# Kernel optimization log

Hardware: AMD Instinct MI355X
Metric: run time of the kernel (lower is better)

## Reference

```python
import jax, jax.numpy as jnp
import numpy as np

INTRA_W, TYPE_W, INTER_W = 1.0, 0.5, 0.5
MARGIN, TAU, EPS = 1.0, 0.1, 1e-8
N, D = 200000, 256          # nodes, feature dim
NT, EPT = 4, 2048           # n types, edges per type
E = NT * EPT                # 8192 hyperedges
SAMP_PER_TYPE = 100         # max_edges_per_type for intra loss
MAX_PAIRS = 500             # inter-loss pair sample


def setup_inputs() -> dict:
    key = jax.random.key(0)
    k1, k2, k3, k4, k5 = jax.random.split(key, 5)
    z_nodes = jax.random.normal(k1, (N, D), dtype=jnp.float32)
    # deterministic variable edge sizes in [8, 56]
    sizes = 8 + (np.arange(E) * 7919) % 49
    M = int(sizes.sum())  # 262128
    member_edge_id = jnp.asarray(np.repeat(np.arange(E), sizes), dtype=jnp.int32)
    member_node_idx = jax.random.randint(k2, (M,), 0, N, dtype=jnp.int32)
    edge_type = jnp.asarray(np.repeat(np.arange(NT), EPT), dtype=jnp.int32)
    # intra-loss edge sampling: 100 edges per type (mimics torch.randperm sampling)
    perm = jax.random.permutation(k3, EPT)
    intra_sample = jnp.concatenate(
        [perm[:SAMP_PER_TYPE] + t * EPT for t in range(NT)]).astype(jnp.int32)
    # inter-loss pair sampling (mimics torch.randint + self-collision fixup)
    pair_idx1 = jax.random.randint(k4, (MAX_PAIRS,), 0, E, dtype=jnp.int32)
    pair_idx2 = jax.random.randint(k5, (MAX_PAIRS,), 0, E, dtype=jnp.int32)
    pair_idx2 = jnp.where(pair_idx1 == pair_idx2, (pair_idx2 + 1) % E, pair_idx2)
    return dict(z_nodes=z_nodes, member_node_idx=member_node_idx,
                member_edge_id=member_edge_id, edge_type=edge_type,
                intra_sample=intra_sample, pair_idx1=pair_idx1, pair_idx2=pair_idx2)


def reference(z_nodes, member_node_idx, member_edge_id, edge_type,
              intra_sample, pair_idx1, pair_idx2):
    # --- ragged segment mean: hyperedge embeddings ---
    gathered = z_nodes[member_node_idx]                               # [M, D]
    counts = jax.ops.segment_sum(jnp.ones_like(member_edge_id, jnp.float32),
                                 member_edge_id, num_segments=E)      # [E]
    edge_sum = jax.ops.segment_sum(gathered, member_edge_id, num_segments=E)
    edge_emb = edge_sum / counts[:, None]                             # [E, D]

    # --- B1: intra-hyperedge loss over sampled edges ---
    sq_dist = jnp.sum((gathered - edge_emb[member_edge_id]) ** 2, axis=-1)  # [M]
    per_edge = jax.ops.segment_sum(sq_dist, member_edge_id, num_segments=E) / counts
    intra = jnp.mean(per_edge[intra_sample])

    # --- B2: type contrastive InfoNCE ---
    z = edge_emb / jnp.linalg.norm(edge_emb, axis=-1, keepdims=True)  # [E, D]
    sim = jnp.matmul(z, z.T) / TAU                                    # [E, E]
    self_mask = jnp.eye(E, dtype=bool)
    exp_sim = jnp.exp(sim) * (~self_mask)
    denom = exp_sim.sum(axis=1)
    type_mask = (edge_type[None, :] == edge_type[:, None]) & ~self_mask
    numer = jnp.sum(exp_sim * type_mask, axis=1)
    per_row = -jnp.log((numer + EPS) / (denom + EPS))
    has_pos = type_mask.sum(axis=1) > 0
    type_loss = jnp.sum(jnp.where(has_pos, per_row, 0.0)) / jnp.maximum(
        has_pos.sum().astype(per_row.dtype), 1.0)

    # --- B3: inter-hyperedge margin loss on sampled pairs ---
    dist = jnp.linalg.norm(edge_emb[pair_idx1] - edge_emb[pair_idx2], axis=-1)
    inter = jnp.mean(jax.nn.relu(MARGIN - dist) ** 2)

    total = INTRA_W * intra + TYPE_W * type_loss + INTER_W * inter
    return jnp.stack([intra, type_loss, inter, total])
```

## Files before the change

### kernel.cpp

```cpp
#include <hip/hip_runtime.h>


#define DDIM 256
#define NTYPES 4
#define TAU_INV 10.0f
#define EPSV 1e-8f

#define ROWS_PER_BLOCK 128
#define ROWS_PER_WAVE 32
#define CHUNK 1024
#define CTILE 64
#define BPAD 264

typedef short v8s __attribute__((ext_vector_type(8)));
typedef float v4f __attribute__((ext_vector_type(4)));
typedef unsigned short ushort_t;

__device__ __forceinline__ int lower_bound_i(const int* __restrict__ a, int n, int key) {
  int lo = 0, hi = n;
  while (lo < hi) { int mid = (lo + hi) >> 1; if (a[mid] < key) lo = mid + 1; else hi = mid; }
  return lo;
}

__device__ __forceinline__ ushort_t f2bf(float f) {
  union { float f; unsigned u; } v; v.f = f;
  unsigned r = v.u + 0x7FFFu + ((v.u >> 16) & 1u);
  return (ushort_t)(r >> 16);
}

__global__ __launch_bounds__(256)
void edge_kernel(const float* __restrict__ z, const int* __restrict__ mni,
                 const int* __restrict__ mei, int M, int E,
                 ushort_t* __restrict__ zn, float* __restrict__ emb,
                 float* __restrict__ per_edge, float* __restrict__ typeSums,
                 float* __restrict__ selfArr, float* __restrict__ scalars) {
  __shared__ int shIdx[64];
  __shared__ float shAcc[1024];
  __shared__ float shRed[12];
  int e = blockIdx.x;
  int tid = threadIdx.x;
  if (tid < NTYPES) typeSums[e * NTYPES + tid] = 0.f;
  if (tid == NTYPES) selfArr[e] = 0.f;
  if (e == 0 && tid >= 16 && tid < 24) scalars[tid - 16] = 0.f;

  int s = lower_bound_i(mei, M, e);
  int t = lower_bound_i(mei, M, e + 1);
  int cnt = t - s;
  if (tid < cnt) shIdx[tid] = mni[s + tid];
  __syncthreads();

  int group = tid >> 6, lane = tid & 63;
  float4 acc = make_float4(0.f, 0.f, 0.f, 0.f);
  float sq = 0.f;
  int m = group;
  for (; m + 4 < cnt; m += 8) {
    int n0 = shIdx[m], n1 = shIdx[m + 4];
    float4 v0 = *(const float4*)(z + (size_t)n0 * DDIM + lane * 4);
    float4 v1 = *(const float4*)(z + (size_t)n1 * DDIM + lane * 4);
    acc.x += v0.x; acc.y += v0.y; acc.z += v0.z; acc.w += v0.w;
    sq += v0.x * v0.x + v0.y * v0.y + v0.z * v0.z + v0.w * v0.w;
    acc.x += v1.x; acc.y += v1.y; acc.z += v1.z; acc.w += v1.w;
    sq += v1.x * v1.x + v1.y * v1.y + v1.z * v1.z + v1.w * v1.w;
  }
  if (m < cnt) {
    int n0 = shIdx[m];
    float4 v0 = *(const float4*)(z + (size_t)n0 * DDIM + lane * 4);
    acc.x += v0.x; acc.y += v0.y; acc.z += v0.z; acc.w += v0.w;
    sq += v0.x * v0.x + v0.y * v0.y + v0.z * v0.z + v0.w * v0.w;
  }

  *(float4*)(&shAcc[tid * 4]) = acc;
  __syncthreads();
  int d = tid;
  float total = shAcc[d] + shAcc[256 + d] + shAcc[512 + d] + shAcc[768 + d];
  float inv = 1.0f / (float)cnt;
  float mu = total * inv;
  emb[(size_t)e * DDIM + d] = mu;

  float a1 = sq, a2 = mu * mu;
  #pragma unroll
  for (int off = 32; off > 0; off >>= 1) {
    a1 += __shfl_down(a1, off);
    a2 += __shfl_down(a2, off);
  }
  if (lane == 0) { shRed[group] = a1; shRed[4 + group] = a2; }
  __syncthreads();
  if (tid == 0) {
    float sqT = shRed[0] + shRed[1] + shRed[2] + shRed[3];
    float musqT = shRed[4] + shRed[5] + shRed[6] + shRed[7];
    per_edge[e] = sqT * inv - musqT;
    shRed[8] = musqT;
  }
  __syncthreads();
  float rn = rsqrtf(shRed[8]);
  zn[(size_t)e * DDIM + d] = f2bf(mu * rn);
}

__global__ __launch_bounds__(256)
void gemm_kernel(const ushort_t* __restrict__ zn, const int* __restrict__ edge_type,
                 int E, float* __restrict__ typeSums, float* __restrict__ selfArr) {
  __shared__ __align__(16) ushort_t sB[CTILE * BPAD];

  int tid = threadIdx.x;
  int lane = tid & 63, wave = tid >> 6;
  int quad = lane >> 4, l15 = lane & 15;
  int rb = blockIdx.y;
  int cb = blockIdx.x;
  int row0 = rb * ROWS_PER_BLOCK + wave * ROWS_PER_WAVE;
  int c0 = cb * CHUNK;
  int T = edge_type[c0];

  v8s aF[2][8];
  #pragma unroll
  for (int rt = 0; rt < 2; ++rt) {
    const ushort_t* base = zn + (size_t)(row0 + rt * 16 + l15) * DDIM + quad * 8;
    #pragma unroll
    for (int ks = 0; ks < 8; ++ks)
      aF[rt][ks] = *(const v8s*)(base + ks * 32);
  }

  float acc[2][4] = {};

  for (int tile = 0; tile < CHUNK / CTILE; ++tile) {
    int col0 = c0 + tile * CTILE;
    #pragma unroll
    for (int it = 0; it < 8; ++it) {
      int flat = it * 256 + tid;
      int r = flat >> 5;
      int c8 = flat & 31;
      *(v8s*)(&sB[r * BPAD + c8 * 8]) =
          *(const v8s*)(zn + (size_t)(col0 + r) * DDIM + c8 * 8);
    }
    __syncthreads();

    v4f c[2][4];
    #pragma unroll
    for (int rt = 0; rt < 2; ++rt)
      #pragma unroll
      for (int ct = 0; ct < 4; ++ct)
        c[rt][ct] = (v4f){0.f, 0.f, 0.f, 0.f};

    #pragma unroll
    for (int ks = 0; ks < 8; ++ks) {
      v8s a0 = aF[0][ks], a1 = aF[1][ks];
      #pragma unroll
      for (int ct = 0; ct < 4; ++ct) {
        v8s b = *(const v8s*)(&sB[(ct * 16 + l15) * BPAD + ks * 32 + quad * 8]);
        c[0][ct] = __builtin_amdgcn_mfma_f32_16x16x32_bf16(a0, b, c[0][ct], 0, 0, 0);
        c[1][ct] = __builtin_amdgcn_mfma_f32_16x16x32_bf16(a1, b, c[1][ct], 0, 0, 0);
      }
    }

    #pragma unroll
    for (int rt = 0; rt < 2; ++rt) {
      #pragma unroll
      for (int ct = 0; ct < 4; ++ct) {
        int col = col0 + ct * 16 + l15;
        #pragma unroll
        for (int r = 0; r < 4; ++r) {
          int row = row0 + rt * 16 + quad * 4 + r;
          float ev = __expf(c[rt][ct][r] * TAU_INV);
          if (col == row) selfArr[row] = ev;
          acc[rt][r] += ev;
        }
      }
    }
    __syncthreads();
  }

  #pragma unroll
  for (int rt = 0; rt < 2; ++rt) {
    #pragma unroll
    for (int r = 0; r < 4; ++r) {
      float v = acc[rt][r];
      v += __shfl_xor(v, 1);
      v += __shfl_xor(v, 2);
      v += __shfl_xor(v, 4);
      v += __shfl_xor(v, 8);
      if (l15 == 0) {
        int row = row0 + rt * 16 + quad * 4 + r;
        atomicAdd(&typeSums[row * NTYPES + T], v);
      }
    }
  }
}

__global__ __launch_bounds__(256)
void small_kernel(const float* __restrict__ emb, const float* __restrict__ per_edge,
                  const int* __restrict__ intra_sample, int nIntra,
                  const int* __restrict__ p1, const int* __restrict__ p2, int nPairs,
                  float* __restrict__ scalars) {
  __shared__ float sh[4];
  int b = blockIdx.x;
  int tid = threadIdx.x;
  int lane = tid & 63, wave = tid >> 6;
  int nPairBlocks = (nPairs + 3) >> 2;
  if (b < nPairBlocks) {
    int p = b * 4 + wave;
    if (p < nPairs) {
      int i1 = p1[p], i2 = p2[p];
      const float4* r1 = (const float4*)(emb + (size_t)i1 * DDIM);
      const float4* r2 = (const float4*)(emb + (size_t)i2 * DDIM);
      float4 x = r1[lane], y = r2[lane];
      float d0 = x.x - y.x, d1 = x.y - y.y, d2 = x.z - y.z, d3 = x.w - y.w;
      float s = d0 * d0 + d1 * d1 + d2 * d2 + d3 * d3;
      #pragma unroll
      for (int off = 32; off > 0; off >>= 1) s += __shfl_down(s, off);
      if (lane == 0) {
        float dist = sqrtf(s);
        float v = fmaxf(1.0f - dist, 0.0f);
        atomicAdd(&scalars[1], v * v);
      }
    }
  } else if (b == nPairBlocks) {
    float s = 0.f;
    for (int i = tid; i < nIntra; i += 256) s += per_edge[intra_sample[i]];
    #pragma unroll
    for (int off = 32; off > 0; off >>= 1) s += __shfl_down(s, off);
    if (lane == 0) sh[wave] = s;
    __syncthreads();
    if (tid == 0) atomicAdd(&scalars[0], sh[0] + sh[1] + sh[2] + sh[3]);
  }
}

__global__ __launch_bounds__(256)
void rowloss_kernel(const float* __restrict__ typeSums, const float* __restrict__ selfArr,
                    const int* __restrict__ edge_type, int E, float* __restrict__ scalars) {
  __shared__ float sh[8];
  int tid = threadIdx.x;
  int row = blockIdx.x * 256 + tid;
  float pr = 0.f, hp = 0.f;
  if (row < E) {
    int t = edge_type[row];
    float self = selfArr[row];
    float s0 = typeSums[row * 4 + 0];
    float s1 = typeSums[row * 4 + 1];
    float s2 = typeSums[row * 4 + 2];
    float s3 = typeSums[row * 4 + 3];
    float denom = (s0 + s1 + s2 + s3) - self;
    float own = (t == 0) ? s0 : (t == 1) ? s1 : (t == 2) ? s2 : s3;
    float numer = own - self;
    int cs = lower_bound_i(edge_type, E, t);
    int ce = lower_bound_i(edge_type, E, t + 1);
    if (ce - cs - 1 > 0) {
      hp = 1.f;
      pr = -__logf((numer + EPSV) / (denom + EPSV));
    }
  }
  float a1 = pr, a2 = hp;
  #pragma unroll
  for (int off = 32; off > 0; off >>= 1) {
    a1 += __shfl_down(a1, off);
    a2 += __shfl_down(a2, off);
  }
  int wid = tid >> 6, lane = tid & 63;
  if (lane == 0) { sh[wid] = a1; sh[4 + wid] = a2; }
  __syncthreads();
  if (tid == 0) {
    atomicAdd(&scalars[2], sh[0] + sh[1] + sh[2] + sh[3]);
    atomicAdd(&scalars[3], sh[4] + sh[5] + sh[6] + sh[7]);
  }
}

__global__ void finalize_kernel(const float* __restrict__ scalars, int nIntra, int nPairs,
                                float* __restrict__ out) {
  if (threadIdx.x == 0) {
    float intra = scalars[0] / (float)nIntra;
    float inter = scalars[1] / (float)nPairs;
    float typeL = scalars[2] / fmaxf(scalars[3], 1.f);
    out[0] = intra;
    out[1] = typeL;
    out[2] = inter;
    out[3] = 1.0f * intra + 0.5f * typeL + 0.5f * inter;
  }
}

extern "C" void kernel_launch(void* const* d_in, const int* in_sizes, int n_in,
                              void* d_out, int out_size, void* d_ws, size_t ws_size,
                              hipStream_t stream) {
  const float* z      = (const float*)d_in[0];
  const int* mni      = (const int*)d_in[1];
  const int* mei      = (const int*)d_in[2];
  const int* etype    = (const int*)d_in[3];
  const int* intra_s  = (const int*)d_in[4];
  const int* p1       = (const int*)d_in[5];
  const int* p2       = (const int*)d_in[6];
  int M      = in_sizes[1];
  int E      = in_sizes[3];
  int nIntra = in_sizes[4];
  int nPairs = in_sizes[5];

  char* ws = (char*)d_ws;
  ushort_t* zn   = (ushort_t*)ws;
  float* emb     = (float*)(ws + (size_t)E * DDIM * 2);
  float* per_edge = (float*)(ws + (size_t)E * DDIM * 6);
  float* typeSums = per_edge + E;
  float* selfArr  = typeSums + (size_t)E * NTYPES;
  float* scalars  = selfArr + E;

  float* out = (float*)d_out;

  edge_kernel<<<E, 256, 0, stream>>>(z, mni, mei, M, E, zn, emb, per_edge,
                                     typeSums, selfArr, scalars);

  dim3 g(E / CHUNK, E / ROWS_PER_BLOCK);
  gemm_kernel<<<g, 256, 0, stream>>>(zn, etype, E, typeSums, selfArr);

  int nPB = (nPairs + 3) / 4;
  small_kernel<<<nPB + 1, 256, 0, stream>>>(emb, per_edge, intra_s, nIntra,
                                            p1, p2, nPairs, scalars);

  rowloss_kernel<<<(E + 255) / 256, 256, 0, stream>>>(typeSums, selfArr, etype, E, scalars);

  finalize_kernel<<<1, 64, 0, stream>>>(scalars, nIntra, nPairs, out);
}
```

Measured before the change: 366.3 us.

## Retile similarity GEMM with double-buffered B, precompute self term, merge tail kernels

```diff
diff --git a/kernel.cpp b/kernel.cpp
--- a/kernel.cpp
+++ b/kernel.cpp
@@ -6,10 +6,9 @@
 #define TAU_INV 10.0f
 #define EPSV 1e-8f
 
-#define ROWS_PER_BLOCK 128
-#define ROWS_PER_WAVE 32
-#define CHUNK 1024
-#define CTILE 64
+#define COLSEG 512
+#define CTILE 32
+#define NTILES (COLSEG / CTILE)
 #define BPAD 264
 
 typedef short v8s __attribute__((ext_vector_type(8)));
@@ -26,6 +25,11 @@
   union { float f; unsigned u; } v; v.f = f;
   unsigned r = v.u + 0x7FFFu + ((v.u >> 16) & 1u);
   return (ushort_t)(r >> 16);
+}
+
+__device__ __forceinline__ float bf2f(ushort_t u) {
+  union { unsigned u; float f; } v; v.u = ((unsigned)u) << 16;
+  return v.f;
 }
 
 __global__ __launch_bounds__(256)
@@ -40,7 +44,6 @@
   int e = blockIdx.x;
   int tid = threadIdx.x;
   if (tid < NTYPES) typeSums[e * NTYPES + tid] = 0.f;
-  if (tid == NTYPES) selfArr[e] = 0.f;
   if (e == 0 && tid >= 16 && tid < 24) scalars[tid - 16] = 0.f;
 
   int s = lower_bound_i(mei, M, e);
@@ -53,16 +56,22 @@
   float4 acc = make_float4(0.f, 0.f, 0.f, 0.f);
   float sq = 0.f;
   int m = group;
-  for (; m + 4 < cnt; m += 8) {
-    int n0 = shIdx[m], n1 = shIdx[m + 4];
+  for (; m + 12 < cnt; m += 16) {
+    int n0 = shIdx[m], n1 = shIdx[m + 4], n2 = shIdx[m + 8], n3 = shIdx[m + 12];
     float4 v0 = *(const float4*)(z + (size_t)n0 * DDIM + lane * 4);
     float4 v1 = *(const float4*)(z + (size_t)n1 * DDIM + lane * 4);
+    float4 v2 = *(const float4*)(z + (size_t)n2 * DDIM + lane * 4);
+    float4 v3 = *(const float4*)(z + (size_t)n3 * DDIM + lane * 4);
     acc.x += v0.x; acc.y += v0.y; acc.z += v0.z; acc.w += v0.w;
     sq += v0.x * v0.x + v0.y * v0.y + v0.z * v0.z + v0.w * v0.w;
     acc.x += v1.x; acc.y += v1.y; acc.z += v1.z; acc.w += v1.w;
     sq += v1.x * v1.x + v1.y * v1.y + v1.z * v1.z + v1.w * v1.w;
-  }
-  if (m < cnt) {
+    acc.x += v2.x; acc.y += v2.y; acc.z += v2.z; acc.w += v2.w;
+    sq += v2.x * v2.x + v2.y * v2.y + v2.z * v2.z + v2.w * v2.w;
+    acc.x += v3.x; acc.y += v3.y; acc.z += v3.z; acc.w += v3.w;
+    sq += v3.x * v3.x + v3.y * v3.y + v3.z * v3.z + v3.w * v3.w;
+  }
+  for (; m < cnt; m += 4) {
     int n0 = shIdx[m];
     float4 v0 = *(const float4*)(z + (size_t)n0 * DDIM + lane * 4);
     acc.x += v0.x; acc.y += v0.y; acc.z += v0.z; acc.w += v0.w;
@@ -93,92 +102,117 @@
   }
   __syncthreads();
   float rn = rsqrtf(shRed[8]);
-  zn[(size_t)e * DDIM + d] = f2bf(mu * rn);
+  ushort_t znv = f2bf(mu * rn);
+  zn[(size_t)e * DDIM + d] = znv;
+
+  float zq = bf2f(znv);
+  float a3 = zq * zq;
+  #pragma unroll
+  for (int off = 32; off > 0; off >>= 1) a3 += __shfl_down(a3, off);
+  if (lane == 0) shRed[group] = a3;
+  __syncthreads();
+  if (tid == 0)
+    selfArr[e] = __expf(TAU_INV * (shRed[0] + shRed[1] + shRed[2] + shRed[3]));
 }
 
 __global__ __launch_bounds__(256)
 void gemm_kernel(const ushort_t* __restrict__ zn, const int* __restrict__ edge_type,
-                 int E, float* __restrict__ typeSums, float* __restrict__ selfArr) {
-  __shared__ __align__(16) ushort_t sB[CTILE * BPAD];
+                 int E, float* __restrict__ typeSums) {
+  __shared__ __align__(16) ushort_t sB[2][CTILE * BPAD];
 
   int tid = threadIdx.x;
   int lane = tid & 63, wave = tid >> 6;
   int quad = lane >> 4, l15 = lane & 15;
   int rb = blockIdx.y;
-  int cb = blockIdx.x;
-  int row0 = rb * ROWS_PER_BLOCK + wave * ROWS_PER_WAVE;
-  int c0 = cb * CHUNK;
+  int cs = blockIdx.x;
+  int row0 = rb * 256 + wave * 64;
+  int c0 = cs * COLSEG;
   int T = edge_type[c0];
 
-  v8s aF[2][8];
-  #pragma unroll
-  for (int rt = 0; rt < 2; ++rt) {
+  v8s aF[4][8];
+  #pragma unroll
+  for (int rt = 0; rt < 4; ++rt) {
     const ushort_t* base = zn + (size_t)(row0 + rt * 16 + l15) * DDIM + quad * 8;
     #pragma unroll
     for (int ks = 0; ks < 8; ++ks)
       aF[rt][ks] = *(const v8s*)(base + ks * 32);
   }
 
-  float acc[2][4] = {};
-
-  for (int tile = 0; tile < CHUNK / CTILE; ++tile) {
-    int col0 = c0 + tile * CTILE;
-    #pragma unroll
-    for (int it = 0; it < 8; ++it) {
-      int flat = it * 256 + tid;
-      int r = flat >> 5;
-      int c8 = flat & 31;
-      *(v8s*)(&sB[r * BPAD + c8 * 8]) =
-          *(const v8s*)(zn + (size_t)(col0 + r) * DDIM + c8 * 8);
+  float acc[4][4] = {};
+
+  v8s r[4];
+  #pragma unroll
+  for (int i = 0; i < 4; ++i) {
+    int id = i * 256 + tid, col = id >> 5, c8 = id & 31;
+    r[i] = *(const v8s*)(zn + (size_t)(c0 + col) * DDIM + c8 * 8);
+  }
+  #pragma unroll
+  for (int i = 0; i < 4; ++i) {
+    int id = i * 256 + tid, col = id >> 5, c8 = id & 31;
+    *(v8s*)(&sB[0][col * BPAD + c8 * 8]) = r[i];
+  }
+  __syncthreads();
+
+  for (int t = 0; t < NTILES; ++t) {
+    v8s rn_[4];
+    if (t < NTILES - 1) {
+      int colb = c0 + (t + 1) * CTILE;
+      #pragma unroll
+      for (int i = 0; i < 4; ++i) {
+        int id = i * 256 + tid, col = id >> 5, c8 = id & 31;
+        rn_[i] = *(const v8s*)(zn + (size_t)(colb + col) * DDIM + c8 * 8);
+      }
+    }
+
+    v4f c[4][2];
+    #pragma unroll
+    for (int rt = 0; rt < 4; ++rt)
+      #pragma unroll
+      for (int ct = 0; ct < 2; ++ct)
+        c[rt][ct] = (v4f){0.f, 0.f, 0.f, 0.f};
+
+    const ushort_t* buf = sB[t & 1];
+    #pragma unroll
+    for (int ks = 0; ks < 8; ++ks) {
+      #pragma unroll
+      for (int ct = 0; ct < 2; ++ct) {
+        v8s b = *(const v8s*)(&buf[(ct * 16 + l15) * BPAD + ks * 32 + quad * 8]);
+        #pragma unroll
+        for (int rt = 0; rt < 4; ++rt)
+          c[rt][ct] = __builtin_amdgcn_mfma_f32_16x16x32_bf16(aF[rt][ks], b, c[rt][ct], 0, 0, 0);
+      }
+    }
+
+    #pragma unroll
+    for (int rt = 0; rt < 4; ++rt)
+      #pragma unroll
+      for (int ct = 0; ct < 2; ++ct)
+        #pragma unroll
+        for (int rr = 0; rr < 4; ++rr)
+          acc[rt][rr] += __expf(c[rt][ct][rr] * TAU_INV);
+
+    if (t < NTILES - 1) {
+      int nb = (t + 1) & 1;
+      #pragma unroll
+      for (int i = 0; i < 4; ++i) {
+        int id = i * 256 + tid, col = id >> 5, c8 = id & 31;
+        *(v8s*)(&sB[nb][col * BPAD + c8 * 8]) = rn_[i];
+      }
     }
     __syncthreads();
-
-    v4f c[2][4];
-    #pragma unroll
-    for (int rt = 0; rt < 2; ++rt)
-      #pragma unroll
-      for (int ct = 0; ct < 4; ++ct)
-        c[rt][ct] = (v4f){0.f, 0.f, 0.f, 0.f};
-
-    #pragma unroll
-    for (int ks = 0; ks < 8; ++ks) {
-      v8s a0 = aF[0][ks], a1 = aF[1][ks];
-      #pragma unroll
-      for (int ct = 0; ct < 4; ++ct) {
-        v8s b = *(const v8s*)(&sB[(ct * 16 + l15) * BPAD + ks * 32 + quad * 8]);
-        c[0][ct] = __builtin_amdgcn_mfma_f32_16x16x32_bf16(a0, b, c[0][ct], 0, 0, 0);
-        c[1][ct] = __builtin_amdgcn_mfma_f32_16x16x32_bf16(a1, b, c[1][ct], 0, 0, 0);
-      }
-    }
-
-    #pragma unroll
-    for (int rt = 0; rt < 2; ++rt) {
-      #pragma unroll
-      for (int ct = 0; ct < 4; ++ct) {
-        int col = col0 + ct * 16 + l15;
-        #pragma unroll
-        for (int r = 0; r < 4; ++r) {
-          int row = row0 + rt * 16 + quad * 4 + r;
-          float ev = __expf(c[rt][ct][r] * TAU_INV);
-          if (col == row) selfArr[row] = ev;
-          acc[rt][r] += ev;
-        }
-      }
-    }
-    __syncthreads();
-  }
-
-  #pragma unroll
-  for (int rt = 0; rt < 2; ++rt) {
-    #pragma unroll
-    for (int r = 0; r < 4; ++r) {
-      float v = acc[rt][r];
+  }
+
+  #pragma unroll
+  for (int rt = 0; rt < 4; ++rt) {
+    #pragma unroll
+    for (int rr = 0; rr < 4; ++rr) {
+      float v = acc[rt][rr];
       v += __shfl_xor(v, 1);
       v += __shfl_xor(v, 2);
       v += __shfl_xor(v, 4);
       v += __shfl_xor(v, 8);
       if (l15 == 0) {
-        int row = row0 + rt * 16 + quad * 4 + r;
+        int row = row0 + rt * 16 + quad * 4 + rr;
         atomicAdd(&typeSums[row * NTYPES + T], v);
       }
     }
@@ -186,51 +220,19 @@
 }
 
 __global__ __launch_bounds__(256)
-void small_kernel(const float* __restrict__ emb, const float* __restrict__ per_edge,
-                  const int* __restrict__ intra_sample, int nIntra,
-                  const int* __restrict__ p1, const int* __restrict__ p2, int nPairs,
-                  float* __restrict__ scalars) {
-  __shared__ float sh[4];
+void tail_kernel(const float* __restrict__ emb, const float* __restrict__ per_edge,
+                 const int* __restrict__ intra_sample, int nIntra,
+                 const int* __restrict__ p1, const int* __restrict__ p2, int nPairs,
+                 const float* __restrict__ typeSums, const float* __restrict__ selfArr,
+                 const int* __restrict__ edge_type, int E, float* __restrict__ scalars) {
+  __shared__ float sh[8];
   int b = blockIdx.x;
   int tid = threadIdx.x;
   int lane = tid & 63, wave = tid >> 6;
-  int nPairBlocks = (nPairs + 3) >> 2;
-  if (b < nPairBlocks) {
-    int p = b * 4 + wave;
-    if (p < nPairs) {
-      int i1 = p1[p], i2 = p2[p];
-      const float4* r1 = (const float4*)(emb + (size_t)i1 * DDIM);
-      const float4* r2 = (const float4*)(emb + (size_t)i2 * DDIM);
-      float4 x = r1[lane], y = r2[lane];
-      float d0 = x.x - y.x, d1 = x.y - y.y, d2 = x.z - y.z, d3 = x.w - y.w;
-      float s = d0 * d0 + d1 * d1 + d2 * d2 + d3 * d3;
-      #pragma unroll
-      for (int off = 32; off > 0; off >>= 1) s += __shfl_down(s, off);
-      if (lane == 0) {
-        float dist = sqrtf(s);
-        float v = fmaxf(1.0f - dist, 0.0f);
-        atomicAdd(&scalars[1], v * v);
-      }
-    }
-  } else if (b == nPairBlocks) {
-    float s = 0.f;
-    for (int i = tid; i < nIntra; i += 256) s += per_edge[intra_sample[i]];
-    #pragma unroll
-    for (int off = 32; off > 0; off >>= 1) s += __shfl_down(s, off);
-    if (lane == 0) sh[wave] = s;
-    __syncthreads();
-    if (tid == 0) atomicAdd(&scalars[0], sh[0] + sh[1] + sh[2] + sh[3]);
-  }
-}
-
-__global__ __launch_bounds__(256)
-void rowloss_kernel(const float* __restrict__ typeSums, const float* __restrict__ selfArr,
-                    const int* __restrict__ edge_type, int E, float* __restrict__ scalars) {
-  __shared__ float sh[8];
-  int tid = threadIdx.x;
-  int row = blockIdx.x * 256 + tid;
-  float pr = 0.f, hp = 0.f;
-  if (row < E) {
+  int nRowBlocks = E / 256;
+
+  if (b < nRowBlocks) {
+    int row = b * 256 + tid;
     int t = edge_type[row];
     float self = selfArr[row];
     float s0 = typeSums[row * 4 + 0];
@@ -240,25 +242,50 @@
     float denom = (s0 + s1 + s2 + s3) - self;
     float own = (t == 0) ? s0 : (t == 1) ? s1 : (t == 2) ? s2 : s3;
     float numer = own - self;
+    float pr = 0.f, hp = 0.f;
     int cs = lower_bound_i(edge_type, E, t);
     int ce = lower_bound_i(edge_type, E, t + 1);
     if (ce - cs - 1 > 0) {
       hp = 1.f;
       pr = -__logf((numer + EPSV) / (denom + EPSV));
     }
-  }
-  float a1 = pr, a2 = hp;
-  #pragma unroll
-  for (int off = 32; off > 0; off >>= 1) {
-    a1 += __shfl_down(a1, off);
-    a2 += __shfl_down(a2, off);
-  }
-  int wid = tid >> 6, lane = tid & 63;
-  if (lane == 0) { sh[wid] = a1; sh[4 + wid] = a2; }
-  __syncthreads();
-  if (tid == 0) {
-    atomicAdd(&scalars[2], sh[0] + sh[1] + sh[2] + sh[3]);
-    atomicAdd(&scalars[3], sh[4] + sh[5] + sh[6] + sh[7]);
+    float a1 = pr, a2 = hp;
+    #pragma unroll
+    for (int off = 32; off > 0; off >>= 1) {
+      a1 += __shfl_down(a1, off);
+      a2 += __shfl_down(a2, off);
+    }
+    if (lane == 0) { sh[wave] = a1; sh[4 + wave] = a2; }
+    __syncthreads();
+    if (tid == 0) {
+      atomicAdd(&scalars[2], sh[0] + sh[1] + sh[2] + sh[3]);
+      atomicAdd(&scalars[3], sh[4] + sh[5] + sh[6] + sh[7]);
+    }
+  } else if (b == nRowBlocks) {
+    float s = 0.f;
+    for (int i = tid; i < nIntra; i += 256) s += per_edge[intra_sample[i]];
+    #pragma unroll
+    for (int off = 32; off > 0; off >>= 1) s += __shfl_down(s, off);
+    if (lane == 0) sh[wave] = s;
+    __syncthreads();
+    if (tid == 0) atomicAdd(&scalars[0], sh[0] + sh[1] + sh[2] + sh[3]);
+  } else {
+    int p = (b - nRowBlocks - 1) * 4 + wave;
+    if (p < nPairs) {
+      int i1 = p1[p], i2 = p2[p];
+      const float4* r1 = (const float4*)(emb + (size_t)i1 * DDIM);
+      const float4* r2 = (const float4*)(emb + (size_t)i2 * DDIM);
+      float4 x = r1[lane], y = r2[lane];
+      float d0 = x.x - y.x, d1 = x.y - y.y, d2 = x.z - y.z, d3 = x.w - y.w;
+      float s = d0 * d0 + d1 * d1 + d2 * d2 + d3 * d3;
+      #pragma unroll
+      for (int off = 32; off > 0; off >>= 1) s += __shfl_down(s, off);
+      if (lane == 0) {
+        float dist = sqrtf(s);
+        float v = fmaxf(1.0f - dist, 0.0f);
+        atomicAdd(&scalars[1], v * v);
+      }
+    }
   }
 }
 
@@ -291,8 +318,8 @@
   int nPairs = in_sizes[5];
 
   char* ws = (char*)d_ws;
-  ushort_t* zn   = (ushort_t*)ws;
-  float* emb     = (float*)(ws + (size_t)E * DDIM * 2);
+  ushort_t* zn    = (ushort_t*)ws;
+  float* emb      = (float*)(ws + (size_t)E * DDIM * 2);
   float* per_edge = (float*)(ws + (size_t)E * DDIM * 6);
   float* typeSums = per_edge + E;
   float* selfArr  = typeSums + (size_t)E * NTYPES;
@@ -303,14 +330,13 @@
   edge_kernel<<<E, 256, 0, stream>>>(z, mni, mei, M, E, zn, emb, per_edge,
                                      typeSums, selfArr, scalars);
 
-  dim3 g(E / CHUNK, E / ROWS_PER_BLOCK);
-  gemm_kernel<<<g, 256, 0, stream>>>(zn, etype, E, typeSums, selfArr);
+  dim3 g(E / COLSEG, E / 256);
+  gemm_kernel<<<g, 256, 0, stream>>>(zn, etype, E, typeSums);
 
   int nPB = (nPairs + 3) / 4;
-  small_kernel<<<nPB + 1, 256, 0, stream>>>(emb, per_edge, intra_s, nIntra,
-                                            p1, p2, nPairs, scalars);
-
-  rowloss_kernel<<<(E + 255) / 256, 256, 0, stream>>>(typeSums, selfArr, etype, E, scalars);
+  tail_kernel<<<E / 256 + 1 + nPB, 256, 0, stream>>>(
+      emb, per_edge, intra_s, nIntra, p1, p2, nPairs,
+      typeSums, selfArr, etype, E, scalars);
 
   finalize_kernel<<<1, 64, 0, stream>>>(scalars, nIntra, nPairs, out);
 }
```

New measurement: 354.7 us. -3.2%, faster.
